# Kernel tuning notes

Hardware: AMD Instinct MI355X
Metric: run time of the kernel (lower is better)

## Reference

```python
import jax, jax.numpy as jnp
import numpy as np

N = 50000          # number of input/output nodes (M == N since out_features=None)
E = 1_600_000      # total neighbor entries (avg degree 32)
C_IN = 64
HID = 128
C_OUT = 64


def setup_inputs() -> dict:
    key = jax.random.key(0)
    k1, k2, k3, k4, k5 = jax.random.split(key, 5)
    in_features = jax.random.normal(k1, (N, C_IN), dtype=jnp.float32)
    # MLP params: Linear(2C->HID), GELU, Linear(HID->C_OUT)
    W1 = jax.random.normal(k2, (2 * C_IN, HID), dtype=jnp.float32) * (1.0 / np.sqrt(2 * C_IN))
    b1 = jnp.zeros((HID,), dtype=jnp.float32)
    W2 = jax.random.normal(k3, (HID, C_OUT), dtype=jnp.float32) * (1.0 / np.sqrt(HID))
    b2 = jnp.zeros((C_OUT,), dtype=jnp.float32)
    neighbors_index = jax.random.randint(k4, (E,), 0, N, dtype=jnp.int64)
    # row_splits: sorted, starts at 0, ends at E (CSR-style ragged offsets)
    inner = jnp.sort(jax.random.randint(k5, (N - 1,), 0, E, dtype=jnp.int64))
    neighbors_row_splits = jnp.concatenate(
        [jnp.zeros((1,), jnp.int64), inner, jnp.full((1,), E, jnp.int64)])
    return {
        "in_features": in_features,
        "W1": W1, "b1": b1, "W2": W2, "b2": b2,
        "neighbors_index": neighbors_index,
        "neighbors_row_splits": neighbors_row_splits,
    }


def reference(in_features, W1, b1, W2, b2, neighbors_index, neighbors_row_splits):
    rs = neighbors_row_splits
    counts = rs[1:] - rs[:-1]                                  # [M] num_reps per row
    # segment id of each edge: row i owns edges [rs[i], rs[i+1])
    seg_ids = jnp.searchsorted(rs[1:], jnp.arange(E), side="right")  # [E]

    rep_features = in_features[neighbors_index]                # gather neighbors [E, C]
    self_features = in_features[seg_ids]                       # repeat_interleave  [E, C]
    agg = jnp.concatenate([rep_features, self_features], axis=1)  # [E, 2C]

    h = jax.nn.gelu(agg @ W1 + b1, approximate=False)          # torch GELU = exact erf
    msg = h @ W2 + b2                                          # [E, C_out]

    summed = jax.ops.segment_sum(msg, seg_ids, num_segments=N)  # [M, C_out]
    denom = jnp.maximum(counts, 1).astype(msg.dtype)[:, None]
    return summed / denom                                       # mean reduction
```

## Files before the change

### kernel.cpp

```cpp
#include <hip/hip_runtime.h>
#include <hip/hip_bf16.h>
#include <math.h>

#define C_IN  64
#define HID   128
#define C_OUT 64

typedef __attribute__((ext_vector_type(8))) short s16x8;
typedef __attribute__((ext_vector_type(4))) float f32x4;
typedef __attribute__((ext_vector_type(2))) float f32x2;

__device__ __forceinline__ f32x2 gelu2(f32x2 x) {
    f32x2 t  = x * x;
    f32x2 p  = t * 0.10294455f + 2.30211462f;
    f32x2 xp = x * p;
    f32x2 E;
    E.x = __builtin_amdgcn_exp2f(xp.x);
    E.y = __builtin_amdgcn_exp2f(xp.y);
    f32x2 Ep = E + 1.0f;
    f32x2 r;
    r.x = __builtin_amdgcn_rcpf(Ep.x);
    r.y = __builtin_amdgcn_rcpf(Ep.y);
    return x - x * r;
}

__device__ __forceinline__ float4 fma4(float s, float4 w, float4 acc) {
    acc.x = fmaf(s, w.x, acc.x); acc.y = fmaf(s, w.y, acc.y);
    acc.z = fmaf(s, w.z, acc.z); acc.w = fmaf(s, w.w, acc.w);
    return acc;
}

__device__ __forceinline__ unsigned pk_bf16(float lo, float hi) {
    union { __hip_bfloat162 v; unsigned u; } cv;
    cv.v = __float22bfloat162_rn(make_float2(lo, hi));
    return cv.u;
}
__device__ __forceinline__ f32x2 unpk2(unsigned p) {
    union { unsigned u; float f; } lo, hi;
    lo.u = p << 16; hi.u = p & 0xffff0000u;
    f32x2 v; v.x = lo.f; v.y = hi.f; return v;
}

#define K1_NODES 64

__global__ __launch_bounds__(512, 2) void precompute_ab(
    const float* __restrict__ X, const float* __restrict__ W1,
    const float* __restrict__ b1, const float* __restrict__ W2,
    unsigned* __restrict__ A16, float* __restrict__ B,
    unsigned short* __restrict__ W2T, int N)
{
    __shared__ float W1s[2 * C_IN * HID];
    __shared__ float xs[K1_NODES * C_IN];
    int tid = threadIdx.x;

    for (int i = tid; i < (2 * C_IN * HID) / 4; i += 512)
        ((float4*)W1s)[i] = ((const float4*)W1)[i];

    int base = blockIdx.x * K1_NODES;
    int nLoc = min(K1_NODES, N - base);
    for (int i = tid; i < nLoc * (C_IN / 4); i += 512)
        ((float4*)xs)[i] = ((const float4*)(X + (size_t)base * C_IN))[i];

    if (blockIdx.x == 0) {
        for (int i = tid; i < C_OUT * HID; i += 512) {
            int c = i >> 7, k = i & (HID - 1);
            W2T[i] = (unsigned short)pk_bf16(W2[k * C_OUT + c], 0.f);
        }
    }
    __syncthreads();

    int quad = (tid & 31) * 4;
    int slot = tid >> 5;
    int s0   = slot * 4;
    if (s0 >= nLoc) return;

    float4 a0 = {}, a1 = {}, a2 = {}, a3 = {};
    float4 b0 = {}, b1r = {}, b2r = {}, b3 = {};

    const float* xr0 = xs + (s0 + 0) * C_IN;
    const float* xr1 = xs + (s0 + 1) * C_IN;
    const float* xr2 = xs + (s0 + 2) * C_IN;
    const float* xr3 = xs + (s0 + 3) * C_IN;

#define K1STEP(c, CMP)                                                      \
    do {                                                                    \
        float4 wa = *(const float4*)&W1s[(c) * HID + quad];                 \
        float4 wb = *(const float4*)&W1s[((c) + C_IN) * HID + quad];        \
        a0 = fma4(xv0.CMP, wa, a0); b0  = fma4(xv0.CMP, wb, b0);            \
        a1 = fma4(xv1.CMP, wa, a1); b1r = fma4(xv1.CMP, wb, b1r);           \
        a2 = fma4(xv2.CMP, wa, a2); b2r = fma4(xv2.CMP, wb, b2r);           \
        a3 = fma4(xv3.CMP, wa, a3); b3  = fma4(xv3.CMP, wb, b3);            \
    } while (0)

#pragma unroll 1
    for (int c4 = 0; c4 < C_IN; c4 += 4) {
        float4 xv0 = *(const float4*)&xr0[c4];
        float4 xv1 = *(const float4*)&xr1[c4];
        float4 xv2 = *(const float4*)&xr2[c4];
        float4 xv3 = *(const float4*)&xr3[c4];
        K1STEP(c4 + 0, x);
        K1STEP(c4 + 1, y);
        K1STEP(c4 + 2, z);
        K1STEP(c4 + 3, w);
    }
#undef K1STEP

    float4 bb = *(const float4*)(b1 + quad);
    b0.x += bb.x;  b0.y += bb.y;  b0.z += bb.z;  b0.w += bb.w;
    b1r.x += bb.x; b1r.y += bb.y; b1r.z += bb.z; b1r.w += bb.w;
    b2r.x += bb.x; b2r.y += bb.y; b2r.z += bb.z; b2r.w += bb.w;
    b3.x += bb.x;  b3.y += bb.y;  b3.z += bb.z;  b3.w += bb.w;

    int adw = (base + s0) * (HID / 2) + (quad >> 1);
    size_t boff = (size_t)(base + s0) * HID + quad;
    if (s0 + 0 < nLoc) {
        uint2 u = { pk_bf16(a0.x, a0.y), pk_bf16(a0.z, a0.w) };
        *(uint2*)(A16 + adw) = u;              *(float4*)(B + boff) = b0;
    }
    if (s0 + 1 < nLoc) {
        uint2 u = { pk_bf16(a1.x, a1.y), pk_bf16(a1.z, a1.w) };
        *(uint2*)(A16 + adw + HID / 2) = u;    *(float4*)(B + boff + HID) = b1r;
    }
    if (s0 + 2 < nLoc) {
        uint2 u = { pk_bf16(a2.x, a2.y), pk_bf16(a2.z, a2.w) };
        *(uint2*)(A16 + adw + HID) = u;        *(float4*)(B + boff + 2 * HID) = b2r;
    }
    if (s0 + 3 < nLoc) {
        uint2 u = { pk_bf16(a3.x, a3.y), pk_bf16(a3.z, a3.w) };
        *(uint2*)(A16 + adw + 3 * (HID / 2)) = u; *(float4*)(B + boff + 3 * HID) = b3;
    }
}

#define EA_WAVES 2

__global__ __launch_bounds__(128) void edge_agg(
    const unsigned* __restrict__ A16, const float* __restrict__ B,
    const int* __restrict__ nbr, const int* __restrict__ rs,
    unsigned* __restrict__ Hout, int N, int E, int G)
{
    int wave = threadIdx.x >> 6, lane = threadIdx.x & 63;
    const unsigned* Al = A16 + lane;
    int b = blockIdx.x;

    int t0 = (int)(((long long)E * b) / G);
    int r0, r1;
    {
        int lo = 0, hi = N;
        while (lo < hi) { int m = (lo + hi) >> 1; if (rs[m] < t0) lo = m + 1; else hi = m; }
        r0 = lo;
    }
    if (b == G - 1) r1 = N;
    else {
        int t1 = (int)(((long long)E * (b + 1)) / G);
        int lo = r0, hi = N;
        while (lo < hi) { int m = (lo + hi) >> 1; if (rs[m] < t1) lo = m + 1; else hi = m; }
        r1 = lo;
    }

    for (int row = r0 + wave; row < r1; row += EA_WAVES) {
        int s = rs[row], e = rs[row + 1];
        int cnt = e - s;

        f32x2 bb = *(const f32x2*)(B + (size_t)row * HID + lane * 2);
        f32x2 acc = {0.f, 0.f};

        int kfull = s + (cnt & ~7);
        int k = s;
        for (; k < kfull; k += 8) {
            int o0 = nbr[k + 0] << 6, o1 = nbr[k + 1] << 6;
            int o2 = nbr[k + 2] << 6, o3 = nbr[k + 3] << 6;
            int o4 = nbr[k + 4] << 6, o5 = nbr[k + 5] << 6;
            int o6 = nbr[k + 6] << 6, o7 = nbr[k + 7] << 6;
            unsigned p0 = Al[o0], p1 = Al[o1], p2 = Al[o2], p3 = Al[o3];
            unsigned p4 = Al[o4], p5 = Al[o5], p6 = Al[o6], p7 = Al[o7];
            acc += gelu2(unpk2(p0) + bb);
            acc += gelu2(unpk2(p1) + bb);
            acc += gelu2(unpk2(p2) + bb);
            acc += gelu2(unpk2(p3) + bb);
            acc += gelu2(unpk2(p4) + bb);
            acc += gelu2(unpk2(p5) + bb);
            acc += gelu2(unpk2(p6) + bb);
            acc += gelu2(unpk2(p7) + bb);
        }
        int rem = e - k;
        if (rem > 4) {
            int e1 = e - 1;
            int o0 = nbr[k + 0] << 6,          o1 = nbr[k + 1] << 6;
            int o2 = nbr[k + 2] << 6,          o3 = nbr[k + 3] << 6;
            int o4 = nbr[min(k + 4, e1)] << 6, o5 = nbr[min(k + 5, e1)] << 6;
            int o6 = nbr[min(k + 6, e1)] << 6, o7 = nbr[min(k + 7, e1)] << 6;
            float m5 = (k + 5 < e) ? 1.f : 0.f, m6 = (k + 6 < e) ? 1.f : 0.f;
            float m7 = (k + 7 < e) ? 1.f : 0.f;
            unsigned p0 = Al[o0], p1 = Al[o1], p2 = Al[o2], p3 = Al[o3];
            unsigned p4 = Al[o4], p5 = Al[o5], p6 = Al[o6], p7 = Al[o7];
            acc += gelu2(unpk2(p0) + bb);
            acc += gelu2(unpk2(p1) + bb);
            acc += gelu2(unpk2(p2) + bb);
            acc += gelu2(unpk2(p3) + bb);
            acc += gelu2(unpk2(p4) + bb);
            acc += gelu2(unpk2(p5) + bb) * m5;
            acc += gelu2(unpk2(p6) + bb) * m6;
            acc += gelu2(unpk2(p7) + bb) * m7;
        } else if (rem > 0) {
            int e1 = e - 1;
            int o0 = nbr[k + 0] << 6,          o1 = nbr[min(k + 1, e1)] << 6;
            int o2 = nbr[min(k + 2, e1)] << 6, o3 = nbr[min(k + 3, e1)] << 6;
            float m1 = (k + 1 < e) ? 1.f : 0.f, m2 = (k + 2 < e) ? 1.f : 0.f;
            float m3 = (k + 3 < e) ? 1.f : 0.f;
            unsigned p0 = Al[o0], p1 = Al[o1], p2 = Al[o2], p3 = Al[o3];
            acc += gelu2(unpk2(p0) + bb);
            acc += gelu2(unpk2(p1) + bb) * m1;
            acc += gelu2(unpk2(p2) + bb) * m2;
            acc += gelu2(unpk2(p3) + bb) * m3;
        }

        float scale = (cnt > 0) ? 1.f / (float)cnt : 0.f;
        Hout[(size_t)row * (HID / 2) + lane] = pk_bf16(acc.x * scale, acc.y * scale);
    }
}

__global__ __launch_bounds__(256) void h_w2_mfma(
    const unsigned short* __restrict__ H, const unsigned short* __restrict__ W2T,
    const float* __restrict__ b2, const int* __restrict__ rs,
    float* __restrict__ out, int N)
{
    int wave = threadIdx.x >> 6, lane = threadIdx.x & 63;
    int base = (blockIdx.x * 4 + wave) * 16;
    if (base >= N) return;

    int r16 = lane & 15;
    int kg  = lane >> 4;

    const unsigned short* hrow = H + (size_t)(base + r16) * HID + kg * 8;
    const unsigned short* wc0  = W2T + (size_t)(0 * 16 + r16) * HID + kg * 8;
    const unsigned short* wc1  = W2T + (size_t)(1 * 16 + r16) * HID + kg * 8;
    const unsigned short* wc2  = W2T + (size_t)(2 * 16 + r16) * HID + kg * 8;
    const unsigned short* wc3  = W2T + (size_t)(3 * 16 + r16) * HID + kg * 8;

    f32x4 acc0 = {0.f, 0.f, 0.f, 0.f};
    f32x4 acc1 = acc0, acc2 = acc0, acc3 = acc0;

#pragma unroll
    for (int kk = 0; kk < 4; ++kk) {
        s16x8 a  = *(const s16x8*)(hrow + kk * 32);
        s16x8 f0 = *(const s16x8*)(wc0 + kk * 32);
        s16x8 f1 = *(const s16x8*)(wc1 + kk * 32);
        s16x8 f2 = *(const s16x8*)(wc2 + kk * 32);
        s16x8 f3 = *(const s16x8*)(wc3 + kk * 32);
        acc0 = __builtin_amdgcn_mfma_f32_16x16x32_bf16(a, f0, acc0, 0, 0, 0);
        acc1 = __builtin_amdgcn_mfma_f32_16x16x32_bf16(a, f1, acc1, 0, 0, 0);
        acc2 = __builtin_amdgcn_mfma_f32_16x16x32_bf16(a, f2, acc2, 0, 0, 0);
        acc3 = __builtin_amdgcn_mfma_f32_16x16x32_bf16(a, f3, acc3, 0, 0, 0);
    }

    float bia0 = b2[r16], bia1 = b2[16 + r16], bia2 = b2[32 + r16], bia3 = b2[48 + r16];

#pragma unroll
    for (int r = 0; r < 4; ++r) {
        int row = base + kg * 4 + r;
        if (row < N) {
            float m = (rs[row + 1] > rs[row]) ? 1.f : 0.f;
            float* o = out + (size_t)row * C_OUT;
            o[r16]      = m * (acc0[r] + bia0);
            o[16 + r16] = m * (acc1[r] + bia1);
            o[32 + r16] = m * (acc2[r] + bia2);
            o[48 + r16] = m * (acc3[r] + bia3);
        }
    }
}

extern "C" void kernel_launch(void* const* d_in, const int* in_sizes, int n_in,
                              void* d_out, int out_size, void* d_ws, size_t ws_size,
                              hipStream_t stream) {
    const float* X  = (const float*)d_in[0];
    const float* W1 = (const float*)d_in[1];
    const float* b1 = (const float*)d_in[2];
    const float* W2 = (const float*)d_in[3];
    const float* b2 = (const float*)d_in[4];
    const int*   nbr = (const int*)d_in[5];
    const int*   rs  = (const int*)d_in[6];
    float* outp = (float*)d_out;

    int N = in_sizes[6] - 1;
    int E = in_sizes[5];

    unsigned*       A16  = (unsigned*)d_ws;
    float*          Bbuf = (float*)(A16 + (size_t)N * (HID / 2));
    unsigned*       Hout = (unsigned*)(Bbuf + (size_t)N * HID);
    unsigned short* W2T  = (unsigned short*)(Hout + (size_t)N * (HID / 2));

    int g1 = (N + K1_NODES - 1) / K1_NODES;
    hipLaunchKernelGGL(precompute_ab, dim3(g1), dim3(512), 0, stream,
                       X, W1, b1, W2, A16, Bbuf, W2T, N);

    int G = 12288;
    hipLaunchKernelGGL(edge_agg, dim3(G), dim3(128), 0, stream,
                       A16, Bbuf, nbr, rs, Hout, N, E, G);

    int stripes = (N + 15) / 16;
    int g3 = (stripes + 3) / 4;
    hipLaunchKernelGGL(h_w2_mfma, dim3(g3), dim3(256), 0, stream,
                       (const unsigned short*)Hout, W2T, b2, rs, outp, N);
}
```

Before: 146.6 us.

## Split wave into half-waves gathering two edges with 8-byte loads and ping-pong prefetch

Rewrites the edge aggregation loop so each wave loads 64 neighbor indices at once and broadcasts them with shuffles. Each half-wave handles a different edge with 8-byte loads covering 4 hidden channels per lane, instead of each lane loading 4 bytes per edge. Gathers for the next group of 8 edges are issued before the current group is processed (double-buffered registers), and the two half-wave accumulators are combined with a cross-half shuffle at the end. The aim is fewer, wider memory instructions and better latency hiding, at the cost of more registers, shuffle overhead and masking logic for partial groups.

```diff
diff --git a/kernel.cpp b/kernel.cpp
--- a/kernel.cpp
+++ b/kernel.cpp
@@ -133,27 +133,58 @@
 
 #define EA_WAVES 2
 
+#define EA_ISSUE(P0,P1,P2,P3, g) do { int _s8 = ((g) << 3) + half;            \
+    int _i0 = __shfl(idx, _s8);                                               \
+    int _i1 = __shfl(idx, _s8 + 2);                                           \
+    int _i2 = __shfl(idx, _s8 + 4);                                           \
+    int _i3 = __shfl(idx, _s8 + 6);                                           \
+    P0 = *(const uint2*)(A8 + ((((unsigned)_i0) << 8) | lb));                 \
+    P1 = *(const uint2*)(A8 + ((((unsigned)_i1) << 8) | lb));                 \
+    P2 = *(const uint2*)(A8 + ((((unsigned)_i2) << 8) | lb));                 \
+    P3 = *(const uint2*)(A8 + ((((unsigned)_i3) << 8) | lb));                 \
+} while (0)
+
+#define EA_PROC1(P) do {                                                      \
+    acc01 += gelu2(unpk2(P.x) + bb01);                                        \
+    acc23 += gelu2(unpk2(P.y) + bb23); } while (0)
+
+#define EA_PROC1M(P, p) do {                                                  \
+    float _mk = ((((p) << 1) + half) < m) ? 1.f : 0.f;                        \
+    acc01 += gelu2(unpk2(P.x) + bb01) * _mk;                                  \
+    acc23 += gelu2(unpk2(P.y) + bb23) * _mk; } while (0)
+
+#define EA_PROCG(P0,P1,P2,P3, g) do {                                         \
+    if ((((g) + 1) << 3) <= m) { EA_PROC1(P0); EA_PROC1(P1);                  \
+                                 EA_PROC1(P2); EA_PROC1(P3); }                \
+    else { int _p = (g) << 2;                                                 \
+           EA_PROC1M(P0, _p);                                                 \
+           if (((_p + 1) << 1) < m) EA_PROC1M(P1, _p + 1);                    \
+           if (((_p + 2) << 1) < m) EA_PROC1M(P2, _p + 2);                    \
+           if (((_p + 3) << 1) < m) EA_PROC1M(P3, _p + 3); } } while (0)
+
 __global__ __launch_bounds__(128) void edge_agg(
     const unsigned* __restrict__ A16, const float* __restrict__ B,
     const int* __restrict__ nbr, const int* __restrict__ rs,
     unsigned* __restrict__ Hout, int N, int E, int G)
 {
     int wave = threadIdx.x >> 6, lane = threadIdx.x & 63;
-    const unsigned* Al = A16 + lane;
+    int half = lane >> 5, l5 = lane & 31;
+    const char* A8 = (const char*)A16;
+    unsigned lb = (unsigned)(l5 << 3);
     int b = blockIdx.x;
 
     int t0 = (int)(((long long)E * b) / G);
     int r0, r1;
     {
         int lo = 0, hi = N;
-        while (lo < hi) { int m = (lo + hi) >> 1; if (rs[m] < t0) lo = m + 1; else hi = m; }
+        while (lo < hi) { int mm = (lo + hi) >> 1; if (rs[mm] < t0) lo = mm + 1; else hi = mm; }
         r0 = lo;
     }
     if (b == G - 1) r1 = N;
     else {
         int t1 = (int)(((long long)E * (b + 1)) / G);
         int lo = r0, hi = N;
-        while (lo < hi) { int m = (lo + hi) >> 1; if (rs[m] < t1) lo = m + 1; else hi = m; }
+        while (lo < hi) { int mm = (lo + hi) >> 1; if (rs[mm] < t1) lo = mm + 1; else hi = mm; }
         r1 = lo;
     }
 
@@ -161,63 +192,48 @@
         int s = rs[row], e = rs[row + 1];
         int cnt = e - s;
 
-        f32x2 bb = *(const f32x2*)(B + (size_t)row * HID + lane * 2);
-        f32x2 acc = {0.f, 0.f};
-
-        int kfull = s + (cnt & ~7);
-        int k = s;
-        for (; k < kfull; k += 8) {
-            int o0 = nbr[k + 0] << 6, o1 = nbr[k + 1] << 6;
-            int o2 = nbr[k + 2] << 6, o3 = nbr[k + 3] << 6;
-            int o4 = nbr[k + 4] << 6, o5 = nbr[k + 5] << 6;
-            int o6 = nbr[k + 6] << 6, o7 = nbr[k + 7] << 6;
-            unsigned p0 = Al[o0], p1 = Al[o1], p2 = Al[o2], p3 = Al[o3];
-            unsigned p4 = Al[o4], p5 = Al[o5], p6 = Al[o6], p7 = Al[o7];
-            acc += gelu2(unpk2(p0) + bb);
-            acc += gelu2(unpk2(p1) + bb);
-            acc += gelu2(unpk2(p2) + bb);
-            acc += gelu2(unpk2(p3) + bb);
-            acc += gelu2(unpk2(p4) + bb);
-            acc += gelu2(unpk2(p5) + bb);
-            acc += gelu2(unpk2(p6) + bb);
-            acc += gelu2(unpk2(p7) + bb);
+        float4 bb4 = *(const float4*)(B + (size_t)row * HID + l5 * 4);
+        f32x2 bb01, bb23;
+        bb01.x = bb4.x; bb01.y = bb4.y; bb23.x = bb4.z; bb23.y = bb4.w;
+        f32x2 acc01 = {0.f, 0.f}, acc23 = {0.f, 0.f};
+
+        for (int cs = s; cs < e; cs += 64) {
+            int m = min(64, e - cs);
+            int idx = nbr[cs + min(lane, m - 1)];
+            int ng = (m + 7) >> 3;
+
+            uint2 A0, A1, A2, A3, B0, B1, B2, B3;
+
+            EA_ISSUE(A0, A1, A2, A3, 0);
+            int g = 0;
+            for (;;) {
+                if (g + 1 < ng) { EA_ISSUE(B0, B1, B2, B3, g + 1);
+                                  EA_PROCG(A0, A1, A2, A3, g); ++g; }
+                else            { EA_PROCG(A0, A1, A2, A3, g); break; }
+                if (g + 1 < ng) { EA_ISSUE(A0, A1, A2, A3, g + 1);
+                                  EA_PROCG(B0, B1, B2, B3, g); ++g; }
+                else            { EA_PROCG(B0, B1, B2, B3, g); break; }
+            }
         }
-        int rem = e - k;
-        if (rem > 4) {
-            int e1 = e - 1;
-            int o0 = nbr[k + 0] << 6,          o1 = nbr[k + 1] << 6;
-            int o2 = nbr[k + 2] << 6,          o3 = nbr[k + 3] << 6;
-            int o4 = nbr[min(k + 4, e1)] << 6, o5 = nbr[min(k + 5, e1)] << 6;
-            int o6 = nbr[min(k + 6, e1)] << 6, o7 = nbr[min(k + 7, e1)] << 6;
-            float m5 = (k + 5 < e) ? 1.f : 0.f, m6 = (k + 6 < e) ? 1.f : 0.f;
-            float m7 = (k + 7 < e) ? 1.f : 0.f;
-            unsigned p0 = Al[o0], p1 = Al[o1], p2 = Al[o2], p3 = Al[o3];
-            unsigned p4 = Al[o4], p5 = Al[o5], p6 = Al[o6], p7 = Al[o7];
-            acc += gelu2(unpk2(p0) + bb);
-            acc += gelu2(unpk2(p1) + bb);
-            acc += gelu2(unpk2(p2) + bb);
-            acc += gelu2(unpk2(p3) + bb);
-            acc += gelu2(unpk2(p4) + bb);
-            acc += gelu2(unpk2(p5) + bb) * m5;
-            acc += gelu2(unpk2(p6) + bb) * m6;
-            acc += gelu2(unpk2(p7) + bb) * m7;
-        } else if (rem > 0) {
-            int e1 = e - 1;
-            int o0 = nbr[k + 0] << 6,          o1 = nbr[min(k + 1, e1)] << 6;
-            int o2 = nbr[min(k + 2, e1)] << 6, o3 = nbr[min(k + 3, e1)] << 6;
-            float m1 = (k + 1 < e) ? 1.f : 0.f, m2 = (k + 2 < e) ? 1.f : 0.f;
-            float m3 = (k + 3 < e) ? 1.f : 0.f;
-            unsigned p0 = Al[o0], p1 = Al[o1], p2 = Al[o2], p3 = Al[o3];
-            acc += gelu2(unpk2(p0) + bb);
-            acc += gelu2(unpk2(p1) + bb) * m1;
-            acc += gelu2(unpk2(p2) + bb) * m2;
-            acc += gelu2(unpk2(p3) + bb) * m3;
+
+        acc01.x += __shfl_xor(acc01.x, 32);
+        acc01.y += __shfl_xor(acc01.y, 32);
+        acc23.x += __shfl_xor(acc23.x, 32);
+        acc23.y += __shfl_xor(acc23.y, 32);
+
+        if (half == 0) {
+            float sc = (cnt > 0) ? 1.f / (float)cnt : 0.f;
+            uint2 o = { pk_bf16(acc01.x * sc, acc01.y * sc),
+                        pk_bf16(acc23.x * sc, acc23.y * sc) };
+            ((uint2*)(Hout + (size_t)row * (HID / 2)))[l5] = o;
         }
-
-        float scale = (cnt > 0) ? 1.f / (float)cnt : 0.f;
-        Hout[(size_t)row * (HID / 2) + lane] = pk_bf16(acc.x * scale, acc.y * scale);
-    }
-}
+    }
+}
+
+#undef EA_ISSUE
+#undef EA_PROC1
+#undef EA_PROC1M
+#undef EA_PROCG
 
 __global__ __launch_bounds__(256) void h_w2_mfma(
     const unsigned short* __restrict__ H, const unsigned short* __restrict__ W2T,
@@ -259,12 +275,12 @@
     for (int r = 0; r < 4; ++r) {
         int row = base + kg * 4 + r;
         if (row < N) {
-            float m = (rs[row + 1] > rs[row]) ? 1.f : 0.f;
+            float mmk = (rs[row + 1] > rs[row]) ? 1.f : 0.f;
             float* o = out + (size_t)row * C_OUT;
-            o[r16]      = m * (acc0[r] + bia0);
-            o[16 + r16] = m * (acc1[r] + bia1);
-            o[32 + r16] = m * (acc2[r] + bia2);
-            o[48 + r16] = m * (acc3[r] + bia3);
+            o[r16]      = mmk * (acc0[r] + bia0);
+            o[16 + r16] = mmk * (acc1[r] + bia1);
+            o[32 + r16] = mmk * (acc2[r] + bia2);
+            o[48 + r16] = mmk * (acc3[r] + bia3);
         }
     }
 }
```

Result: faster. 133.9 us (-8.7%).
